# Kernel optimization log

Measured on AMD Instinct MI355X. Metric: run time of the kernel, lower is better.

The kernel has to match this reference:

```python
import jax, jax.numpy as jnp
import numpy as np

B, N, T, D = 32, 1024, 64, 32  # latent_dim = D


def setup_inputs() -> dict:
    key = jax.random.key(0)
    ks = jax.random.split(key, 12)
    s = 0.1
    return {
        "spatial_nodes": jax.random.normal(ks[0], (B, N, D), jnp.float32),
        "temporal_nodes": jax.random.normal(ks[1], (B, T, D), jnp.float32),
        # st MLP: Linear(2D -> D), Sigmoid, Linear(D -> 1). Weights stored (in, out).
        "st_w1": jax.random.normal(ks[2], (2 * D, D), jnp.float32) * s,
        "st_b1": jax.random.normal(ks[3], (D,), jnp.float32) * s,
        "st_w2": jax.random.normal(ks[4], (D, 1), jnp.float32) * s,
        "st_b2": jax.random.normal(ks[5], (1,), jnp.float32) * s,
        "ts_w1": jax.random.normal(ks[6], (2 * D, D), jnp.float32) * s,
        "ts_b1": jax.random.normal(ks[7], (D,), jnp.float32) * s,
        "ts_w2": jax.random.normal(ks[8], (D, 1), jnp.float32) * s,
        "ts_b2": jax.random.normal(ks[9], (1,), jnp.float32) * s,
    }


def _sub_graph(x1, x2, w1, b1, w2, b2):
    # Faithful to Linear(concat(x1_tile, x2_tile)) but without materializing
    # the tiled/concatenated [B, N1, N2, 2D] tensor: split w1 by input half.
    d = x1.shape[-1]
    a = x1 @ w1[:d]          # [B, N1, D]
    b = x2 @ w1[d:]          # [B, N2, D]
    h = jax.nn.sigmoid(a[:, :, None, :] + b[:, None, :, :] + b1)  # [B, N1, N2, D]
    return jnp.einsum('bnmd,do->bnm', h, w2) + b2[0]               # [B, N1, N2]


def reference(spatial_nodes, temporal_nodes,
              st_w1, st_b1, st_w2, st_b2,
              ts_w1, ts_b1, ts_w2, ts_b2):
    n = spatial_nodes.shape[1]
    node_embs = jnp.concatenate([spatial_nodes, temporal_nodes], axis=1)  # [B, N+T, D]
    adj = jnp.einsum('bnf,bmf->bnm', node_embs, node_embs)                # [B, N+T, N+T]
    st_adj = _sub_graph(spatial_nodes, temporal_nodes, st_w1, st_b1, st_w2, st_b2)
    ts_adj = _sub_graph(temporal_nodes, spatial_nodes, ts_w1, ts_b1, ts_w2, ts_b2)
    adj = adj.at[:, :n, n:].set(st_adj)
    adj = adj.at[:, n:, :n].set(ts_adj)
    adj = jnp.tanh(jax.nn.relu(adj))
    return adj
```

## Files before the change

### kernel.cpp

```cpp
#include <hip/hip_runtime.h>

namespace {
constexpr int kB = 32;
constexpr int kN = 1024;
constexpr int kT = 64;
constexpr int kD = 32;
constexpr int kM = 1088;

constexpr int BLK_ST = kB * 16;
constexpr int BLK_TS = kB * 16;
constexpr int BLK_TT = kB;
constexpr int BLK_NN = kB * 8 * 8;
constexpr int OFF_TT = BLK_ST + BLK_TS;
constexpr int OFF_NN = OFF_TT + BLK_TT;
constexpr int BLK_TOTAL = OFF_NN + BLK_NN;

struct SMemGram128 { float A[128][36]; float Bt[32][132]; };
struct SMemGram64  { float A[64][36];  float Bt[32][68];  };
struct SMemMLP {
  union {
    struct { float raw1[64][36]; float raw2[64][36]; } r;
    struct { float EA[64][36]; float EBt[32][68]; } e;
  } u;
  float w1[64][32];
  float w2v[32];
  float b1v[32];
  float b2v;
};
union SMem { SMemGram128 g; SMemGram64 g64; SMemMLP m; };
}

#define FMA4(ACC, AV, B, C)            \
  ACC = fmaf(AV.x, B[0].C, ACC);       \
  ACC = fmaf(AV.y, B[1].C, ACC);       \
  ACC = fmaf(AV.z, B[2].C, ACC);       \
  ACC = fmaf(AV.w, B[3].C, ACC);

#define SIGSTEP(AROW, EAV, EBD, W2D)                                            \
  AROW[0] = fmaf(W2D, __builtin_amdgcn_rcpf(fmaf(EAV, EBD.x, 1.f)), AROW[0]);   \
  AROW[1] = fmaf(W2D, __builtin_amdgcn_rcpf(fmaf(EAV, EBD.y, 1.f)), AROW[1]);   \
  AROW[2] = fmaf(W2D, __builtin_amdgcn_rcpf(fmaf(EAV, EBD.z, 1.f)), AROW[2]);   \
  AROW[3] = fmaf(W2D, __builtin_amdgcn_rcpf(fmaf(EAV, EBD.w, 1.f)), AROW[3]);

__device__ __forceinline__ float tanh_relu(float x) {
  const float xp = fmaxf(x, 0.f);
  const float e = __expf(2.f * xp);
  return 1.f - 2.f * __builtin_amdgcn_rcpf(e + 1.f);
}

__global__ void __launch_bounds__(256)
adj_kernel(const float* __restrict__ sp, const float* __restrict__ tp,
           const float* __restrict__ st_w1, const float* __restrict__ st_b1,
           const float* __restrict__ st_w2, const float* __restrict__ st_b2,
           const float* __restrict__ ts_w1, const float* __restrict__ ts_b1,
           const float* __restrict__ ts_w2, const float* __restrict__ ts_b2,
           float* __restrict__ out) {
  __shared__ SMem sm;
  const int bid = blockIdx.x;
  const int tid = threadIdx.x;
  const int tx = tid & 15;
  const int ty = tid >> 4;

  if (bid >= OFF_NN) {
    const int bid2 = bid - OFF_NN;
    const int b = bid2 >> 6;
    const int t = bid2 & 63;
    const int r0 = (t >> 3) * 128;
    const int c0 = (t & 7) * 128;
    const float* rowp = sp + ((size_t)b * kN + r0) * kD;
    const float* colp = sp + ((size_t)b * kN + c0) * kD;
    for (int q = tid; q < 1024; q += 256) {
      const int r = q >> 3, c = (q & 7) * 4;
      *(float4*)&sm.g.A[r][c] = ((const float4*)rowp)[q];
      const float4 w = ((const float4*)colp)[q];
      sm.g.Bt[c + 0][r] = w.x;
      sm.g.Bt[c + 1][r] = w.y;
      sm.g.Bt[c + 2][r] = w.z;
      sm.g.Bt[c + 3][r] = w.w;
    }
    __syncthreads();
    float acc[8][8] = {};
    #pragma unroll
    for (int k4 = 0; k4 < 8; ++k4) {
      float4 b0[4], b1[4];
      #pragma unroll
      for (int kk = 0; kk < 4; ++kk) {
        b0[kk] = *(const float4*)&sm.g.Bt[k4 * 4 + kk][tx * 4];
        b1[kk] = *(const float4*)&sm.g.Bt[k4 * 4 + kk][64 + tx * 4];
      }
      #pragma unroll
      for (int i = 0; i < 8; ++i) {
        const int row = (i & 4) * 16 + ty * 4 + (i & 3);
        const float4 a = *(const float4*)&sm.g.A[row][k4 * 4];
        FMA4(acc[i][0], a, b0, x)
        FMA4(acc[i][1], a, b0, y)
        FMA4(acc[i][2], a, b0, z)
        FMA4(acc[i][3], a, b0, w)
        FMA4(acc[i][4], a, b1, x)
        FMA4(acc[i][5], a, b1, y)
        FMA4(acc[i][6], a, b1, z)
        FMA4(acc[i][7], a, b1, w)
      }
    }
    const size_t base = (size_t)b * kM * kM + (size_t)c0 + tx * 4;
    #pragma unroll
    for (int i = 0; i < 8; ++i) {
      const int r = r0 + (i & 4) * 16 + ty * 4 + (i & 3);
      float4 o0, o1;
      o0.x = tanh_relu(acc[i][0]); o0.y = tanh_relu(acc[i][1]);
      o0.z = tanh_relu(acc[i][2]); o0.w = tanh_relu(acc[i][3]);
      o1.x = tanh_relu(acc[i][4]); o1.y = tanh_relu(acc[i][5]);
      o1.z = tanh_relu(acc[i][6]); o1.w = tanh_relu(acc[i][7]);
      *(float4*)&out[base + (size_t)r * kM] = o0;
      *(float4*)&out[base + (size_t)r * kM + 64] = o1;
    }
  } else if (bid >= OFF_TT) {
    const int b = bid - OFF_TT;
    const float* rowp = tp + (size_t)b * kT * kD;
    for (int q = tid; q < 512; q += 256) {
      const int r = q >> 3, c = (q & 7) * 4;
      const float4 v = ((const float4*)rowp)[q];
      *(float4*)&sm.g64.A[r][c] = v;
      sm.g64.Bt[c + 0][r] = v.x;
      sm.g64.Bt[c + 1][r] = v.y;
      sm.g64.Bt[c + 2][r] = v.z;
      sm.g64.Bt[c + 3][r] = v.w;
    }
    __syncthreads();
    float acc[4][4] = {};
    #pragma unroll
    for (int k4 = 0; k4 < 8; ++k4) {
      float4 b4[4];
      #pragma unroll
      for (int kk = 0; kk < 4; ++kk)
        b4[kk] = *(const float4*)&sm.g64.Bt[k4 * 4 + kk][tx * 4];
      #pragma unroll
      for (int i = 0; i < 4; ++i) {
        const float4 a = *(const float4*)&sm.g64.A[ty * 4 + i][k4 * 4];
        FMA4(acc[i][0], a, b4, x)
        FMA4(acc[i][1], a, b4, y)
        FMA4(acc[i][2], a, b4, z)
        FMA4(acc[i][3], a, b4, w)
      }
    }
    const size_t base = (size_t)b * kM * kM + (size_t)kN + tx * 4;
    #pragma unroll
    for (int i = 0; i < 4; ++i) {
      const int r = kN + ty * 4 + i;
      float4 o;
      o.x = tanh_relu(acc[i][0]);
      o.y = tanh_relu(acc[i][1]);
      o.z = tanh_relu(acc[i][2]);
      o.w = tanh_relu(acc[i][3]);
      *(float4*)&out[base + (size_t)r * kM] = o;
    }
  } else {
    int b, r0, c0;
    const float *rowp, *colp, *w1, *b1, *w2, *b2;
    if (bid < BLK_ST) {
      b = bid >> 4;
      r0 = (bid & 15) * 64; c0 = kN;
      rowp = sp + ((size_t)b * kN + r0) * kD;
      colp = tp + (size_t)b * kT * kD;
      w1 = st_w1; b1 = st_b1; w2 = st_w2; b2 = st_b2;
    } else {
      const int i = bid - BLK_ST;
      b = i >> 4;
      r0 = kN; c0 = (i & 15) * 64;
      rowp = tp + (size_t)b * kT * kD;
      colp = sp + ((size_t)b * kN + c0) * kD;
      w1 = ts_w1; b1 = ts_b1; w2 = ts_w2; b2 = ts_b2;
    }
    for (int q = tid; q < 512; q += 256) {
      const int r = q >> 3, c = (q & 7) * 4;
      *(float4*)&sm.m.u.r.raw1[r][c] = ((const float4*)rowp)[q];
      *(float4*)&sm.m.u.r.raw2[r][c] = ((const float4*)colp)[q];
      ((float4*)sm.m.w1)[q] = ((const float4*)w1)[q];
    }
    if (tid < kD) { sm.m.w2v[tid] = w2[tid]; sm.m.b1v[tid] = b1[tid]; }
    if (tid == 0) sm.m.b2v = b2[0];
    __syncthreads();
    const int pr = tid >> 2;
    const int d0 = (tid & 3) * 8;
    float pa[8], pb[8];
    #pragma unroll
    for (int q = 0; q < 8; ++q) { pa[q] = 0.f; pb[q] = sm.m.b1v[d0 + q]; }
    for (int k = 0; k < kD; ++k) {
      const float s1 = sm.m.u.r.raw1[pr][k];
      const float s2 = sm.m.u.r.raw2[pr][k];
      const float4 wa0 = *(const float4*)&sm.m.w1[k][d0];
      const float4 wa1 = *(const float4*)&sm.m.w1[k][d0 + 4];
      const float4 wb0 = *(const float4*)&sm.m.w1[kD + k][d0];
      const float4 wb1 = *(const float4*)&sm.m.w1[kD + k][d0 + 4];
      pa[0] = fmaf(s1, wa0.x, pa[0]); pa[1] = fmaf(s1, wa0.y, pa[1]);
      pa[2] = fmaf(s1, wa0.z, pa[2]); pa[3] = fmaf(s1, wa0.w, pa[3]);
      pa[4] = fmaf(s1, wa1.x, pa[4]); pa[5] = fmaf(s1, wa1.y, pa[5]);
      pa[6] = fmaf(s1, wa1.z, pa[6]); pa[7] = fmaf(s1, wa1.w, pa[7]);
      pb[0] = fmaf(s2, wb0.x, pb[0]); pb[1] = fmaf(s2, wb0.y, pb[1]);
      pb[2] = fmaf(s2, wb0.z, pb[2]); pb[3] = fmaf(s2, wb0.w, pb[3]);
      pb[4] = fmaf(s2, wb1.x, pb[4]); pb[5] = fmaf(s2, wb1.y, pb[5]);
      pb[6] = fmaf(s2, wb1.z, pb[6]); pb[7] = fmaf(s2, wb1.w, pb[7]);
    }
    const float b2s = sm.m.b2v;
    __syncthreads();
    #pragma unroll
    for (int q = 0; q < 8; ++q) {
      sm.m.u.e.EA[pr][d0 + q] = __expf(-pa[q]);
      sm.m.u.e.EBt[d0 + q][pr] = __expf(-pb[q]);
    }
    __syncthreads();
    float acc[4][4];
    #pragma unroll
    for (int ii = 0; ii < 4; ++ii) {
      acc[ii][0] = b2s; acc[ii][1] = b2s; acc[ii][2] = b2s; acc[ii][3] = b2s;
    }
    #pragma unroll
    for (int d4 = 0; d4 < 8; ++d4) {
      float4 ea[4];
      #pragma unroll
      for (int ii = 0; ii < 4; ++ii)
        ea[ii] = *(const float4*)&sm.m.u.e.EA[ty * 4 + ii][d4 * 4];
      const float4 eb0 = *(const float4*)&sm.m.u.e.EBt[d4 * 4 + 0][tx * 4];
      const float4 eb1 = *(const float4*)&sm.m.u.e.EBt[d4 * 4 + 1][tx * 4];
      const float4 eb2 = *(const float4*)&sm.m.u.e.EBt[d4 * 4 + 2][tx * 4];
      const float4 eb3 = *(const float4*)&sm.m.u.e.EBt[d4 * 4 + 3][tx * 4];
      const float w20 = sm.m.w2v[d4 * 4 + 0];
      const float w21 = sm.m.w2v[d4 * 4 + 1];
      const float w22 = sm.m.w2v[d4 * 4 + 2];
      const float w23 = sm.m.w2v[d4 * 4 + 3];
      #pragma unroll
      for (int ii = 0; ii < 4; ++ii) {
        SIGSTEP(acc[ii], ea[ii].x, eb0, w20)
        SIGSTEP(acc[ii], ea[ii].y, eb1, w21)
        SIGSTEP(acc[ii], ea[ii].z, eb2, w22)
        SIGSTEP(acc[ii], ea[ii].w, eb3, w23)
      }
    }
    const size_t base = (size_t)b * kM * kM + (size_t)c0 + tx * 4;
    #pragma unroll
    for (int ii = 0; ii < 4; ++ii) {
      const int r = r0 + ty * 4 + ii;
      float4 o;
      o.x = tanh_relu(acc[ii][0]);
      o.y = tanh_relu(acc[ii][1]);
      o.z = tanh_relu(acc[ii][2]);
      o.w = tanh_relu(acc[ii][3]);
      *(float4*)&out[base + (size_t)r * kM] = o;
    }
  }
}

extern "C" void kernel_launch(void* const* d_in, const int* in_sizes, int n_in,
                              void* d_out, int out_size, void* d_ws, size_t ws_size,
                              hipStream_t stream) {
  const float* sp    = (const float*)d_in[0];
  const float* tp    = (const float*)d_in[1];
  const float* st_w1 = (const float*)d_in[2];
  const float* st_b1 = (const float*)d_in[3];
  const float* st_w2 = (const float*)d_in[4];
  const float* st_b2 = (const float*)d_in[5];
  const float* ts_w1 = (const float*)d_in[6];
  const float* ts_b1 = (const float*)d_in[7];
  const float* ts_w2 = (const float*)d_in[8];
  const float* ts_b2 = (const float*)d_in[9];
  float* out = (float*)d_out;
  (void)in_sizes; (void)n_in; (void)out_size; (void)d_ws; (void)ws_size;
  adj_kernel<<<dim3(BLK_TOTAL), dim3(256), 0, stream>>>(
      sp, tp, st_w1, st_b1, st_w2, st_b2, ts_w1, ts_b1, ts_w2, ts_b2, out);
}
```

Measured before the change: 203.4 us.

## Exploit Gram matrix symmetry: compute upper-triangle tiles and write transposed copies

The spatial-spatial Gram block is symmetric, so only the 36 upper-triangular 128x128 tiles per batch are computed instead of 64. Off-diagonal tiles also write their transpose through a shared-memory staging buffer, so the mirrored output is produced without recomputing the dot products. This roughly halves the Gram FLOPs and input loads. In exchange it adds a loop-based tile index decode, extra syncs and LDS transposes, and more store work per block. Total output bytes are unchanged, which matters because the kernel is likely bound by output writes.

```diff
diff --git a/kernel.cpp b/kernel.cpp
--- a/kernel.cpp
+++ b/kernel.cpp
@@ -10,10 +10,10 @@
 constexpr int BLK_ST = kB * 16;
 constexpr int BLK_TS = kB * 16;
 constexpr int BLK_TT = kB;
-constexpr int BLK_NN = kB * 8 * 8;
+constexpr int BLK_NNS = kB * 36;
 constexpr int OFF_TT = BLK_ST + BLK_TS;
 constexpr int OFF_NN = OFF_TT + BLK_TT;
-constexpr int BLK_TOTAL = OFF_NN + BLK_NN;
+constexpr int BLK_TOTAL = OFF_NN + BLK_NNS;
 
 struct SMemGram128 { float A[128][36]; float Bt[32][132]; };
 struct SMemGram64  { float A[64][36];  float Bt[32][68];  };
@@ -27,7 +27,7 @@
   float b1v[32];
   float b2v;
 };
-union SMem { SMemGram128 g; SMemGram64 g64; SMemMLP m; };
+union SMem { SMemGram128 g; SMemGram64 g64; SMemMLP m; float tr[64][132]; };
 }
 
 #define FMA4(ACC, AV, B, C)            \
@@ -63,10 +63,13 @@
 
   if (bid >= OFF_NN) {
     const int bid2 = bid - OFF_NN;
-    const int b = bid2 >> 6;
-    const int t = bid2 & 63;
-    const int r0 = (t >> 3) * 128;
-    const int c0 = (t & 7) * 128;
+    const int b = bid2 / 36;
+    int rem = bid2 - b * 36;
+    int ti = 0;
+    while (rem >= 8 - ti) { rem -= 8 - ti; ++ti; }
+    const int tj = ti + rem;
+    const int r0 = ti * 128;
+    const int c0 = tj * 128;
     const float* rowp = sp + ((size_t)b * kN + r0) * kD;
     const float* colp = sp + ((size_t)b * kN + c0) * kD;
     for (int q = tid; q < 1024; q += 256) {
@@ -102,17 +105,44 @@
         FMA4(acc[i][7], a, b1, w)
       }
     }
+    #pragma unroll
+    for (int i = 0; i < 8; ++i) {
+      acc[i][0] = tanh_relu(acc[i][0]); acc[i][1] = tanh_relu(acc[i][1]);
+      acc[i][2] = tanh_relu(acc[i][2]); acc[i][3] = tanh_relu(acc[i][3]);
+      acc[i][4] = tanh_relu(acc[i][4]); acc[i][5] = tanh_relu(acc[i][5]);
+      acc[i][6] = tanh_relu(acc[i][6]); acc[i][7] = tanh_relu(acc[i][7]);
+    }
     const size_t base = (size_t)b * kM * kM + (size_t)c0 + tx * 4;
     #pragma unroll
     for (int i = 0; i < 8; ++i) {
       const int r = r0 + (i & 4) * 16 + ty * 4 + (i & 3);
       float4 o0, o1;
-      o0.x = tanh_relu(acc[i][0]); o0.y = tanh_relu(acc[i][1]);
-      o0.z = tanh_relu(acc[i][2]); o0.w = tanh_relu(acc[i][3]);
-      o1.x = tanh_relu(acc[i][4]); o1.y = tanh_relu(acc[i][5]);
-      o1.z = tanh_relu(acc[i][6]); o1.w = tanh_relu(acc[i][7]);
+      o0.x = acc[i][0]; o0.y = acc[i][1]; o0.z = acc[i][2]; o0.w = acc[i][3];
+      o1.x = acc[i][4]; o1.y = acc[i][5]; o1.z = acc[i][6]; o1.w = acc[i][7];
       *(float4*)&out[base + (size_t)r * kM] = o0;
       *(float4*)&out[base + (size_t)r * kM + 64] = o1;
+    }
+    if (ti != tj) {
+      #pragma unroll
+      for (int g = 0; g < 2; ++g) {
+        __syncthreads();
+        #pragma unroll
+        for (int i = 0; i < 8; ++i) {
+          const int r = (i & 4) * 16 + ty * 4 + (i & 3);
+          sm.tr[tx * 4 + 0][r] = acc[i][g * 4 + 0];
+          sm.tr[tx * 4 + 1][r] = acc[i][g * 4 + 1];
+          sm.tr[tx * 4 + 2][r] = acc[i][g * 4 + 2];
+          sm.tr[tx * 4 + 3][r] = acc[i][g * 4 + 3];
+        }
+        __syncthreads();
+        const int cl = tid >> 2;
+        const int off = (tid & 3) * 32;
+        const size_t obase = (size_t)b * kM * kM +
+                             (size_t)(c0 + g * 64 + cl) * kM + r0 + off;
+        #pragma unroll
+        for (int q = 0; q < 8; ++q)
+          *(float4*)&out[obase + q * 4] = *(const float4*)&sm.tr[cl][off + q * 4];
+      }
     }
   } else if (bid >= OFF_TT) {
     const int b = bid - OFF_TT;
```

After: 206.1 us. No clear change (+1.3%).
